# Kernel tuning notes

Hardware: AMD Instinct MI355X
Metric: run time of the kernel (lower is better)

## Reference

```python
import jax, jax.numpy as jnp
import numpy as np

N_NODES = 100000
N_EDGES = 1600000
IN_CH = 128
HID = 128
EPS = 1e-5


def setup_inputs() -> dict:
    key = jax.random.key(0)
    ks = jax.random.split(key, 16)
    x = jax.random.normal(ks[0], (N_NODES, IN_CH), dtype=jnp.float32)
    edge_index = jax.random.randint(ks[1], (2, N_EDGES), 0, N_NODES, dtype=jnp.int64)
    dims = [(IN_CH, HID), (HID, HID), (HID, HID // 2)]
    params = {}
    for i, (di, do) in enumerate(dims):
        params[f'w{i}'] = jax.random.normal(ks[2 + i], (di, do), dtype=jnp.float32) * (1.0 / np.sqrt(di))
        params[f'b{i}'] = jnp.zeros((do,), dtype=jnp.float32)
        params[f'g{i}'] = jnp.ones((do,), dtype=jnp.float32)
        params[f'be{i}'] = jnp.zeros((do,), dtype=jnp.float32)
    params['wc1'] = jax.random.normal(ks[8], (HID // 2, 32), dtype=jnp.float32) * (1.0 / np.sqrt(HID // 2))
    params['bc1'] = jnp.zeros((32,), dtype=jnp.float32)
    params['wc2'] = jax.random.normal(ks[9], (32, 1), dtype=jnp.float32) * (1.0 / np.sqrt(32))
    params['bc2'] = jnp.zeros((1,), dtype=jnp.float32)
    return {'x': x, 'edge_index': edge_index, **params}


def _gcn_forward(x, edge_index, w0, b0, g0, be0, w1, b1, g1, be1, w2, b2, g2, be2, wc1, bc1, wc2, bc2):
    n = x.shape[0]
    # add self-loops (GCNConv default)
    loops = jnp.arange(n, dtype=edge_index.dtype)
    src = jnp.concatenate([edge_index[0], loops])  # [E+N]
    dst = jnp.concatenate([edge_index[1], loops])
    # symmetric normalization: deg over targets (incl. self loops)
    deg = jax.ops.segment_sum(jnp.ones_like(dst, dtype=x.dtype), dst, num_segments=n)
    dis = jax.lax.rsqrt(jnp.maximum(deg, 1e-12))  # deg>=1 due to self loops
    norm = (dis[src] * dis[dst])[:, None]  # [E+N, 1]

    def layer(h, w, b, g, be):
        h = h @ w                                   # [N, d_out]
        h = jax.ops.segment_sum(h[src] * norm, dst, num_segments=n) + b
        mu = jnp.mean(h, axis=0)
        var = jnp.mean(jnp.square(h - mu), axis=0)  # biased var (torch BN)
        h = (h - mu) * jax.lax.rsqrt(var + EPS) * g + be
        return jax.nn.relu(h)                       # dropout: identity (eval)

    h = layer(x, w0, b0, g0, be0)
    h = layer(h, w1, b1, g1, be1)
    h = layer(h, w2, b2, g2, be2)
    h = jax.nn.relu(h @ wc1 + bc1)
    return (h @ wc2 + bc2)[:, 0]  # [N]


def reference(x, edge_index, w0, b0, g0, be0, w1, b1, g1, be1, w2, b2, g2, be2, wc1, bc1, wc2, bc2):
    return _gcn_forward(x, edge_index, w0, b0, g0, be0, w1, b1, g1, be1, w2, b2, g2, be2, wc1, bc1, wc2, bc2)
```

## Files before the change

kernel.cpp:

```cpp
#include <hip/hip_runtime.h>


typedef __attribute__((ext_vector_type(8))) short short8;
typedef __attribute__((ext_vector_type(4))) float f32x4;

#define BIN_SHIFT 7
#define BIN_NODES 128
#define CAPB 4096
#define SUBCAP 512
#define CAP 64
#define SPARTS 1024

__device__ __forceinline__ float b2f(unsigned short u) {
    return __uint_as_float(((unsigned)u) << 16);
}
__device__ __forceinline__ unsigned short f2bf(float f) {
    unsigned u = __float_as_uint(f);
    return (unsigned short)((u + 0x7fff + ((u >> 16) & 1)) >> 16);
}

__global__ __launch_bounds__(256) void part1_kernel(const int* __restrict__ eidx,
                                                    int E, int nbins, int chunk,
                                                    int* __restrict__ bin_fill,
                                                    int* __restrict__ binned) {
    __shared__ int cntS[1024];
    __shared__ int baseS[1024];
    int tid = threadIdx.x;
    int sub = blockIdx.x & 7;
    for (int b = tid; b < nbins; b += 256) cntS[b] = 0;
    __syncthreads();
    int e0 = blockIdx.x * chunk;
    int e1 = min(e0 + chunk, E);
    for (int e = e0 + tid; e < e1; e += 256)
        atomicAdd(&cntS[eidx[E + e] >> BIN_SHIFT], 1);
    __syncthreads();
    for (int b = tid; b < nbins; b += 256) {
        baseS[b] = atomicAdd(&bin_fill[b * 8 + sub], cntS[b]);
        cntS[b] = 0;
    }
    __syncthreads();
    for (int e = e0 + tid; e < e1; e += 256) {
        int d = eidx[E + e];
        int s = eidx[e];
        int b = d >> BIN_SHIFT;
        int p = baseS[b] + atomicAdd(&cntS[b], 1);
        if (p < SUBCAP)
            binned[b * CAPB + sub * SUBCAP + p] = (s << BIN_SHIFT) | (d & (BIN_NODES - 1));
    }
}

__global__ __launch_bounds__(256) void part2_kernel(const int* __restrict__ bin_fill,
                                                    const int* __restrict__ binned,
                                                    int N, int* __restrict__ fill,
                                                    float* __restrict__ dis,
                                                    int* __restrict__ stage) {
    __shared__ int lfill[BIN_NODES];
    int b = blockIdx.x, tid = threadIdx.x;
    if (tid < BIN_NODES) lfill[tid] = 0;
    __syncthreads();
    for (int sub = 0; sub < 8; sub++) {
        int cnt = min(bin_fill[b * 8 + sub], SUBCAP);
        const int* seg = binned + b * CAPB + sub * SUBCAP;
        for (int i = tid; i < cnt; i += 256) {
            int v = seg[i];
            int dl = v & (BIN_NODES - 1);
            int p = atomicAdd(&lfill[dl], 1);
            int node = (b << BIN_SHIFT) + dl;
            if (p < CAP) stage[(node << 6) + p] = v >> BIN_SHIFT;
        }
    }
    __syncthreads();
    if (tid < BIN_NODES) {
        int node = (b << BIN_SHIFT) + tid;
        if (node < N) {
            int c = lfill[tid];
            fill[node] = c;
            dis[node] = rsqrtf((float)c + 1.0f);
        }
    }
}

__global__ void wfrag_kernel(const float* __restrict__ w0,
                             const float* __restrict__ w1,
                             const float* __restrict__ w2,
                             unsigned short* __restrict__ wf) {
    int tid = blockIdx.x * 256 + threadIdx.x;
    if (tid >= 40960) return;
    const float* w;
    int idx, C;
    if (tid < 16384) { w = w0; idx = tid; C = 128; }
    else if (tid < 32768) { w = w1; idx = tid - 16384; C = 128; }
    else { w = w2; idx = tid - 32768; C = 64; }
    int j = idx & 7;
    int lane = (idx >> 3) & 63;
    int q = (idx >> 9) & 3;
    int n_tile = idx >> 11;
    int k = q * 32 + (lane >> 4) * 8 + j;
    int n = n_tile * 16 + (lane & 15);
    wf[tid] = f2bf(w[k * C + n]);
}

__device__ __forceinline__ void load8(const float* p, float4& lo, float4& hi) {
    lo = *(const float4*)p;
    hi = *(const float4*)(p + 4);
}
__device__ __forceinline__ void load8(const unsigned short* p, float4& lo, float4& hi) {
    int4 q = *(const int4*)p;
    lo = make_float4(__uint_as_float((unsigned)q.x << 16),
                     __uint_as_float((unsigned)q.x & 0xffff0000u),
                     __uint_as_float((unsigned)q.y << 16),
                     __uint_as_float((unsigned)q.y & 0xffff0000u));
    hi = make_float4(__uint_as_float((unsigned)q.z << 16),
                     __uint_as_float((unsigned)q.z & 0xffff0000u),
                     __uint_as_float((unsigned)q.w << 16),
                     __uint_as_float((unsigned)q.w & 0xffff0000u));
}

template <int C, typename InT>
__global__ __launch_bounds__(256, 5) void mfma_gemm_kernel(
    const InT* __restrict__ xin, const unsigned short* __restrict__ wf,
    const float* __restrict__ scale, const float* __restrict__ shift,
    const float* __restrict__ dis, unsigned short* __restrict__ out, int N) {
    constexpr int NT = C / 16;
    constexpr int WFRAGS = NT * 4 * 64;
    __shared__ short8 ws[WFRAGS];
    int tid = threadIdx.x;
    for (int i = tid; i < WFRAGS; i += 256) ws[i] = ((const short8*)wf)[i];

    int lane = tid & 63;
    int wave = tid >> 6;
    int m0 = blockIdx.x * 64 + wave * 16;
    int r15 = lane & 15, r4 = lane >> 4;
    f32x4 acc[NT];
#pragma unroll
    for (int t = 0; t < NT; t++) acc[t] = (f32x4){0.f, 0.f, 0.f, 0.f};
    int row0 = m0 + r15;
    int row0c = min(row0, N - 1);
    __syncthreads();

#pragma unroll
    for (int q = 0; q < 4; q++) {
        int kb = q * 32 + r4 * 8;
        float4 a0l, a0h;
        load8(xin + (size_t)row0c * 128 + kb, a0l, a0h);
        if (scale) {
            float4 scl = *(const float4*)&scale[kb];
            float4 sch = *(const float4*)&scale[kb + 4];
            float4 shl = *(const float4*)&shift[kb];
            float4 shh = *(const float4*)&shift[kb + 4];
            a0l.x = fmaxf(a0l.x * scl.x + shl.x, 0.f);
            a0l.y = fmaxf(a0l.y * scl.y + shl.y, 0.f);
            a0l.z = fmaxf(a0l.z * scl.z + shl.z, 0.f);
            a0l.w = fmaxf(a0l.w * scl.w + shl.w, 0.f);
            a0h.x = fmaxf(a0h.x * sch.x + shh.x, 0.f);
            a0h.y = fmaxf(a0h.y * sch.y + shh.y, 0.f);
            a0h.z = fmaxf(a0h.z * sch.z + shh.z, 0.f);
            a0h.w = fmaxf(a0h.w * sch.w + shh.w, 0.f);
        }
        short8 a0;
        a0[0] = (short)f2bf(a0l.x); a0[1] = (short)f2bf(a0l.y);
        a0[2] = (short)f2bf(a0l.z); a0[3] = (short)f2bf(a0l.w);
        a0[4] = (short)f2bf(a0h.x); a0[5] = (short)f2bf(a0h.y);
        a0[6] = (short)f2bf(a0h.z); a0[7] = (short)f2bf(a0h.w);
#pragma unroll
        for (int nt = 0; nt < NT; nt++) {
            short8 b = ws[(nt * 4 + q) * 64 + lane];
            acc[nt] = __builtin_amdgcn_mfma_f32_16x16x32_bf16(a0, b, acc[nt], 0, 0, 0);
        }
    }
    float d0r[4];
#pragma unroll
    for (int r = 0; r < 4; r++) {
        int rowa = m0 + r4 * 4 + r;
        d0r[r] = (rowa < N) ? dis[rowa] : 0.f;
    }
#pragma unroll
    for (int nt = 0; nt < NT; nt++) {
        int col = nt * 16 + r15;
#pragma unroll
        for (int r = 0; r < 4; r++) {
            int rowa = m0 + r4 * 4 + r;
            if (rowa < N) out[(size_t)rowa * C + col] = f2bf(acc[nt][r] * d0r[r]);
        }
    }
}

__global__ __launch_bounds__(256) void agg128_kernel(
    const unsigned short* __restrict__ h, const int* __restrict__ fill,
    const int* __restrict__ stage, const float* __restrict__ dis,
    unsigned short* __restrict__ out, int N) {
    int lane = threadIdx.x & 63;
    int node = blockIdx.x * 4 + (threadIdx.x >> 6);
    if (node >= N) return;
    float dn = dis[node];
    ushort2 sv = ((const ushort2*)(h + (size_t)node * 128))[lane];
    float2 acc = make_float2(b2f(sv.x), b2f(sv.y));
    int ne = min(fill[node], CAP);
    int pk = (lane < ne) ? stage[(node << 6) + lane] : 0;
    int j = 0;
    for (; j + 16 <= ne; j += 16) {
        ushort2 a[16];
#pragma unroll
        for (int t = 0; t < 16; t++) {
            int s = __builtin_amdgcn_readlane(pk, j + t);
            a[t] = ((const ushort2*)(h + (size_t)s * 128))[lane];
        }
#pragma unroll
        for (int t = 0; t < 16; t++) { acc.x += b2f(a[t].x); acc.y += b2f(a[t].y); }
    }
    for (; j + 8 <= ne; j += 8) {
        ushort2 a[8];
#pragma unroll
        for (int t = 0; t < 8; t++) {
            int s = __builtin_amdgcn_readlane(pk, j + t);
            a[t] = ((const ushort2*)(h + (size_t)s * 128))[lane];
        }
#pragma unroll
        for (int t = 0; t < 8; t++) { acc.x += b2f(a[t].x); acc.y += b2f(a[t].y); }
    }
    for (; j + 4 <= ne; j += 4) {
        ushort2 a[4];
#pragma unroll
        for (int t = 0; t < 4; t++) {
            int s = __builtin_amdgcn_readlane(pk, j + t);
            a[t] = ((const ushort2*)(h + (size_t)s * 128))[lane];
        }
#pragma unroll
        for (int t = 0; t < 4; t++) { acc.x += b2f(a[t].x); acc.y += b2f(a[t].y); }
    }
    for (; j < ne; j++) {
        int s = __builtin_amdgcn_readlane(pk, j);
        ushort2 a = ((const ushort2*)(h + (size_t)s * 128))[lane];
        acc.x += b2f(a.x);
        acc.y += b2f(a.y);
    }
    ((ushort2*)(out + (size_t)node * 128))[lane] =
        make_ushort2(f2bf(acc.x * dn), f2bf(acc.y * dn));
}

__global__ __launch_bounds__(256) void agg64_kernel(
    const unsigned short* __restrict__ h, const int* __restrict__ fill,
    const int* __restrict__ stage, const float* __restrict__ dis,
    unsigned short* __restrict__ out, int N) {
    int lane = threadIdx.x & 63;
    int node = blockIdx.x * 4 + (threadIdx.x >> 6);
    if (node >= N) return;
    int half = lane >> 5, ch = lane & 31;
    float dn = dis[node];
    float2 acc = make_float2(0.f, 0.f);
    if (half == 0) {
        ushort2 sv = ((const ushort2*)(h + (size_t)node * 64))[ch];
        acc.x = b2f(sv.x);
        acc.y = b2f(sv.y);
    }
    int ne = min(fill[node], CAP);
    int pk = (lane < ne) ? stage[(node << 6) + lane] : 0;
    int j = 0;
    for (; j + 16 <= ne; j += 16) {
        ushort2 a[8];
#pragma unroll
        for (int t = 0; t < 8; t++) {
            int s = __shfl(pk, j + 2 * t + half);
            a[t] = ((const ushort2*)(h + (size_t)s * 64))[ch];
        }
#pragma unroll
        for (int t = 0; t < 8; t++) { acc.x += b2f(a[t].x); acc.y += b2f(a[t].y); }
    }
    for (; j + 8 <= ne; j += 8) {
        ushort2 a[4];
#pragma unroll
        for (int t = 0; t < 4; t++) {
            int s = __shfl(pk, j + 2 * t + half);
            a[t] = ((const ushort2*)(h + (size_t)s * 64))[ch];
        }
#pragma unroll
        for (int t = 0; t < 4; t++) { acc.x += b2f(a[t].x); acc.y += b2f(a[t].y); }
    }
    for (; j < ne; j += 2) {
        int jj = j + half;
        int s = __shfl(pk, jj);
        bool v = jj < ne;
        ushort2 a = ((const ushort2*)(h + (size_t)s * 64))[ch];
        acc.x += v ? b2f(a.x) : 0.f;
        acc.y += v ? b2f(a.y) : 0.f;
    }
    acc.x += __shfl_down(acc.x, 32);
    acc.y += __shfl_down(acc.y, 32);
    if (half == 0)
        ((ushort2*)(out + (size_t)node * 64))[ch] =
            make_ushort2(f2bf(acc.x * dn), f2bf(acc.y * dn));
}

template <int C>
__global__ __launch_bounds__(256) void stats1_kernel(const unsigned short* __restrict__ h,
                                                     int N, float* __restrict__ partials) {
    constexpr int CG = C / 4;
    constexpr int RG = 256 / CG;
    int t = threadIdx.x;
    int cg = t % CG;
    int rg = t / CG;
    float s[4] = {0.f, 0.f, 0.f, 0.f}, q[4] = {0.f, 0.f, 0.f, 0.f};
    for (int n = blockIdx.x * RG + rg; n < N; n += gridDim.x * RG) {
        ushort4 v = *(const ushort4*)&h[(size_t)n * C + cg * 4];
        float f0 = b2f(v.x), f1 = b2f(v.y), f2 = b2f(v.z), f3 = b2f(v.w);
        s[0] += f0; s[1] += f1; s[2] += f2; s[3] += f3;
        q[0] += f0 * f0; q[1] += f1 * f1; q[2] += f2 * f2; q[3] += f3 * f3;
    }
    __shared__ float red[256 * 8];
#pragma unroll
    for (int k = 0; k < 4; k++) {
        red[(rg * CG + cg) * 8 + k] = s[k];
        red[(rg * CG + cg) * 8 + 4 + k] = q[k];
    }
    __syncthreads();
    if (rg == 0) {
#pragma unroll
        for (int w = 1; w < RG; w++)
#pragma unroll
            for (int k = 0; k < 4; k++) {
                s[k] += red[(w * CG + cg) * 8 + k];
                q[k] += red[(w * CG + cg) * 8 + 4 + k];
            }
        float* pb = partials + (size_t)blockIdx.x * 2 * C;
#pragma unroll
        for (int k = 0; k < 4; k++) {
            pb[cg * 4 + k] = s[k];
            pb[C + cg * 4 + k] = q[k];
        }
    }
}

template <int C>
__global__ __launch_bounds__(256) void stats2_kernel(const float* __restrict__ partials,
                                                     const float* __restrict__ g,
                                                     const float* __restrict__ be, int N,
                                                     float* __restrict__ scale,
                                                     float* __restrict__ shift) {
    int c = blockIdx.x;
    int t = threadIdx.x;
    float s = 0.f, q = 0.f;
    for (int b = t; b < SPARTS; b += 256) {
        const float* pb = partials + (size_t)b * 2 * C;
        s += pb[c];
        q += pb[C + c];
    }
    __shared__ float rs[256], rq[256];
    rs[t] = s;
    rq[t] = q;
    __syncthreads();
    for (int d = 128; d > 0; d >>= 1) {
        if (t < d) {
            rs[t] += rs[t + d];
            rq[t] += rq[t + d];
        }
        __syncthreads();
    }
    if (t == 0) {
        float inv_n = 1.0f / (float)N;
        float mean = rs[0] * inv_n;
        float var = rq[0] * inv_n - mean * mean;
        var = var > 0.f ? var : 0.f;
        float sc = g[c] * rsqrtf(var + 1e-5f);
        scale[c] = sc;
        shift[c] = be[c] - mean * sc;
    }
}

__global__ __launch_bounds__(256) void head_kernel(
    const unsigned short* __restrict__ h, const float* __restrict__ scale,
    const float* __restrict__ shift, const float* __restrict__ wc1,
    const float* __restrict__ bc1, const float* __restrict__ wc2,
    const float* __restrict__ bc2, float* __restrict__ out, int N) {
    __shared__ float w1s[64 * 32];
    __shared__ float b1s[32], w2s[32], s2s[64], sh2[64];
    __shared__ float b2s;
    int tid = threadIdx.x;
    for (int i = tid; i < 64 * 32; i += 256) w1s[i] = wc1[i];
    if (tid < 32) { b1s[tid] = bc1[tid]; w2s[tid] = wc2[tid]; }
    if (tid < 64) { s2s[tid] = scale[tid]; sh2[tid] = shift[tid]; }
    if (tid == 0) b2s = bc2[0];
    __syncthreads();
    int n = blockIdx.x * 256 + tid;
    if (n >= N) return;
    float v[64];
#pragma unroll
    for (int k = 0; k < 64; k++) {
        float x = b2f(h[(size_t)n * 64 + k]) * s2s[k] + sh2[k];
        v[k] = x > 0.f ? x : 0.f;
    }
    float o = b2s;
#pragma unroll 2
    for (int j = 0; j < 32; j++) {
        float t = b1s[j];
#pragma unroll
        for (int k = 0; k < 64; k++) t += v[k] * w1s[k * 32 + j];
        t = t > 0.f ? t : 0.f;
        o += t * w2s[j];
    }
    out[n] = o;
}

extern "C" void kernel_launch(void* const* d_in, const int* in_sizes, int n_in,
                              void* d_out, int out_size, void* d_ws, size_t ws_size,
                              hipStream_t stream) {
    const float* x = (const float*)d_in[0];
    const int* eidx = (const int*)d_in[1];
    const float* w0 = (const float*)d_in[2];
    const float* g0 = (const float*)d_in[4];
    const float* be0 = (const float*)d_in[5];
    const float* w1 = (const float*)d_in[6];
    const float* g1 = (const float*)d_in[8];
    const float* be1 = (const float*)d_in[9];
    const float* w2 = (const float*)d_in[10];
    const float* g2 = (const float*)d_in[12];
    const float* be2 = (const float*)d_in[13];
    const float* wc1 = (const float*)d_in[14];
    const float* bc1 = (const float*)d_in[15];
    const float* wc2 = (const float*)d_in[16];
    const float* bc2 = (const float*)d_in[17];

    const int N = in_sizes[0] / 128;
    const int E = in_sizes[1] / 2;
    const int nbins = (N + BIN_NODES - 1) >> BIN_SHIFT;

    char* p = (char*)d_ws;
    auto alloc = [&](size_t bytes) {
        void* r = (void*)p;
        p += (bytes + 255) & ~(size_t)255;
        return r;
    };
    int* bin_fill = (int*)alloc((size_t)nbins * 8 * 4);
    size_t zero_bytes = (size_t)(p - (char*)d_ws);
    int* fill = (int*)alloc((size_t)N * 4);
    int* binned = (int*)alloc((size_t)nbins * CAPB * 4);
    int* stage = (int*)alloc((size_t)N * CAP * 4);
    float* dis = (float*)alloc((size_t)N * 4);
    float* ss = (float*)alloc(3 * 256 * 4);
    float* partials = (float*)alloc((size_t)SPARTS * 256 * 4);
    unsigned short* hA = (unsigned short*)alloc((size_t)N * 128 * 2);
    unsigned short* hB = (unsigned short*)alloc((size_t)N * 128 * 2);
    unsigned short* wf = (unsigned short*)alloc(40960 * 2);
    unsigned short* wf0 = wf;
    unsigned short* wf1 = wf + 16384;
    unsigned short* wf2 = wf + 32768;

    float* sc0 = ss, *sh0 = ss + 128;
    float* sc1 = ss + 256, *sh1 = ss + 384;
    float* sc2 = ss + 512, *sh2 = ss + 640;

    hipMemsetAsync(d_ws, 0, zero_bytes, stream);

    wfrag_kernel<<<160, 256, 0, stream>>>(w0, w1, w2, wf);
    int p1_blocks = 256;
    int chunk = (E + p1_blocks - 1) / p1_blocks;
    part1_kernel<<<p1_blocks, 256, 0, stream>>>(eidx, E, nbins, chunk, bin_fill, binned);
    part2_kernel<<<nbins, 256, 0, stream>>>(bin_fill, binned, N, fill, dis, stage);

    int agg_grid = (N + 3) / 4;
    int gemm_grid = (N + 63) / 64;

    mfma_gemm_kernel<128, float><<<gemm_grid, 256, 0, stream>>>(x, wf0, nullptr, nullptr,
                                                                dis, hA, N);
    agg128_kernel<<<agg_grid, 256, 0, stream>>>(hA, fill, stage, dis, hB, N);
    stats1_kernel<128><<<SPARTS, 256, 0, stream>>>(hB, N, partials);
    stats2_kernel<128><<<128, 256, 0, stream>>>(partials, g0, be0, N, sc0, sh0);

    mfma_gemm_kernel<128, unsigned short><<<gemm_grid, 256, 0, stream>>>(
        hB, wf1, sc0, sh0, dis, hA, N);
    agg128_kernel<<<agg_grid, 256, 0, stream>>>(hA, fill, stage, dis, hB, N);
    stats1_kernel<128><<<SPARTS, 256, 0, stream>>>(hB, N, partials);
    stats2_kernel<128><<<128, 256, 0, stream>>>(partials, g1, be1, N, sc1, sh1);

    mfma_gemm_kernel<64, unsigned short><<<gemm_grid, 256, 0, stream>>>(
        hB, wf2, sc1, sh1, dis, hA, N);
    agg64_kernel<<<agg_grid, 256, 0, stream>>>(hA, fill, stage, dis, hB, N);
    stats1_kernel<64><<<SPARTS, 256, 0, stream>>>(hB, N, partials);
    stats2_kernel<64><<<64, 256, 0, stream>>>(partials, g2, be2, N, sc2, sh2);

    head_kernel<<<(N + 255) / 256, 256, 0, stream>>>(hB, sc2, sh2, wc1, bc1, wc2,
                                                     bc2, (float*)d_out, N);
}
```

Before: 435.4 us.

## Merge prep kernels, fuse BN stats reduction via last-block counter, widen agg blocks

Merges the weight-fragment conversion into the edge binning kernel as extra blocks, and fuses the two-pass BN statistics reduction into a single kernel in which the last block to finish (tracked by an atomic counter) does the final reduction. This removes several kernel launches. The partial count drops from 1024 to 256, aggregation blocks grow from 4 to 8 nodes (512 threads), and the head kernel now loads its bf16 input in vector chunks. The final reduction runs serially per channel in one block, and the fused stats step relies on threadfence ordering being correct.

Result: slower. 517.8 us (+18.9%).

```diff
diff --git a/kernel.cpp b/kernel.cpp
--- a/kernel.cpp
+++ b/kernel.cpp
@@ -9,7 +9,7 @@
 #define CAPB 4096
 #define SUBCAP 512
 #define CAP 64
-#define SPARTS 1024
+#define SPARTS 256
 
 __device__ __forceinline__ float b2f(unsigned short u) {
     return __uint_as_float(((unsigned)u) << 16);
@@ -19,17 +19,36 @@
     return (unsigned short)((u + 0x7fff + ((u >> 16) & 1)) >> 16);
 }
 
-__global__ __launch_bounds__(256) void part1_kernel(const int* __restrict__ eidx,
-                                                    int E, int nbins, int chunk,
-                                                    int* __restrict__ bin_fill,
-                                                    int* __restrict__ binned) {
+__global__ __launch_bounds__(256) void prep_kernel(
+    const float* __restrict__ w0, const float* __restrict__ w1,
+    const float* __restrict__ w2, unsigned short* __restrict__ wf,
+    const int* __restrict__ eidx, int E, int nbins, int chunk,
+    int* __restrict__ bin_fill, int* __restrict__ binned) {
     __shared__ int cntS[1024];
     __shared__ int baseS[1024];
+    if (blockIdx.x < 160) {
+        int tid = blockIdx.x * 256 + threadIdx.x;
+        if (tid >= 40960) return;
+        const float* w;
+        int idx, C;
+        if (tid < 16384) { w = w0; idx = tid; C = 128; }
+        else if (tid < 32768) { w = w1; idx = tid - 16384; C = 128; }
+        else { w = w2; idx = tid - 32768; C = 64; }
+        int j = idx & 7;
+        int lane = (idx >> 3) & 63;
+        int q = (idx >> 9) & 3;
+        int n_tile = idx >> 11;
+        int k = q * 32 + (lane >> 4) * 8 + j;
+        int n = n_tile * 16 + (lane & 15);
+        wf[tid] = f2bf(w[k * C + n]);
+        return;
+    }
+    int blk = blockIdx.x - 160;
     int tid = threadIdx.x;
-    int sub = blockIdx.x & 7;
+    int sub = blk & 7;
     for (int b = tid; b < nbins; b += 256) cntS[b] = 0;
     __syncthreads();
-    int e0 = blockIdx.x * chunk;
+    int e0 = blk * chunk;
     int e1 = min(e0 + chunk, E);
     for (int e = e0 + tid; e < e1; e += 256)
         atomicAdd(&cntS[eidx[E + e] >> BIN_SHIFT], 1);
@@ -78,26 +97,6 @@
             dis[node] = rsqrtf((float)c + 1.0f);
         }
     }
-}
-
-__global__ void wfrag_kernel(const float* __restrict__ w0,
-                             const float* __restrict__ w1,
-                             const float* __restrict__ w2,
-                             unsigned short* __restrict__ wf) {
-    int tid = blockIdx.x * 256 + threadIdx.x;
-    if (tid >= 40960) return;
-    const float* w;
-    int idx, C;
-    if (tid < 16384) { w = w0; idx = tid; C = 128; }
-    else if (tid < 32768) { w = w1; idx = tid - 16384; C = 128; }
-    else { w = w2; idx = tid - 32768; C = 64; }
-    int j = idx & 7;
-    int lane = (idx >> 3) & 63;
-    int q = (idx >> 9) & 3;
-    int n_tile = idx >> 11;
-    int k = q * 32 + (lane >> 4) * 8 + j;
-    int n = n_tile * 16 + (lane & 15);
-    wf[tid] = f2bf(w[k * C + n]);
 }
 
 __device__ __forceinline__ void load8(const float* p, float4& lo, float4& hi) {
@@ -185,12 +184,12 @@
     }
 }
 
-__global__ __launch_bounds__(256) void agg128_kernel(
+__global__ __launch_bounds__(512) void agg128_kernel(
     const unsigned short* __restrict__ h, const int* __restrict__ fill,
     const int* __restrict__ stage, const float* __restrict__ dis,
     unsigned short* __restrict__ out, int N) {
     int lane = threadIdx.x & 63;
-    int node = blockIdx.x * 4 + (threadIdx.x >> 6);
+    int node = blockIdx.x * 8 + (threadIdx.x >> 6);
     if (node >= N) return;
     float dn = dis[node];
     ushort2 sv = ((const ushort2*)(h + (size_t)node * 128))[lane];
@@ -238,12 +237,12 @@
         make_ushort2(f2bf(acc.x * dn), f2bf(acc.y * dn));
 }
 
-__global__ __launch_bounds__(256) void agg64_kernel(
+__global__ __launch_bounds__(512) void agg64_kernel(
     const unsigned short* __restrict__ h, const int* __restrict__ fill,
     const int* __restrict__ stage, const float* __restrict__ dis,
     unsigned short* __restrict__ out, int N) {
     int lane = threadIdx.x & 63;
-    int node = blockIdx.x * 4 + (threadIdx.x >> 6);
+    int node = blockIdx.x * 8 + (threadIdx.x >> 6);
     if (node >= N) return;
     int half = lane >> 5, ch = lane & 31;
     float dn = dis[node];
@@ -292,15 +291,18 @@
 }
 
 template <int C>
-__global__ __launch_bounds__(256) void stats1_kernel(const unsigned short* __restrict__ h,
-                                                     int N, float* __restrict__ partials) {
+__global__ __launch_bounds__(256) void stats_kernel(
+    const unsigned short* __restrict__ h, int N, float* __restrict__ partials,
+    unsigned int* __restrict__ counter, const float* __restrict__ g,
+    const float* __restrict__ be, float* __restrict__ scale,
+    float* __restrict__ shift) {
     constexpr int CG = C / 4;
     constexpr int RG = 256 / CG;
     int t = threadIdx.x;
     int cg = t % CG;
     int rg = t / CG;
     float s[4] = {0.f, 0.f, 0.f, 0.f}, q[4] = {0.f, 0.f, 0.f, 0.f};
-    for (int n = blockIdx.x * RG + rg; n < N; n += gridDim.x * RG) {
+    for (int n = blockIdx.x * RG + rg; n < N; n += SPARTS * RG) {
         ushort4 v = *(const ushort4*)&h[(size_t)n * C + cg * 4];
         float f0 = b2f(v.x), f1 = b2f(v.y), f2 = b2f(v.z), f3 = b2f(v.w);
         s[0] += f0; s[1] += f1; s[2] += f2; s[3] += f3;
@@ -328,41 +330,29 @@
             pb[C + cg * 4 + k] = q[k];
         }
     }
-}
-
-template <int C>
-__global__ __launch_bounds__(256) void stats2_kernel(const float* __restrict__ partials,
-                                                     const float* __restrict__ g,
-                                                     const float* __restrict__ be, int N,
-                                                     float* __restrict__ scale,
-                                                     float* __restrict__ shift) {
-    int c = blockIdx.x;
-    int t = threadIdx.x;
-    float s = 0.f, q = 0.f;
-    for (int b = t; b < SPARTS; b += 256) {
-        const float* pb = partials + (size_t)b * 2 * C;
-        s += pb[c];
-        q += pb[C + c];
-    }
-    __shared__ float rs[256], rq[256];
-    rs[t] = s;
-    rq[t] = q;
-    __syncthreads();
-    for (int d = 128; d > 0; d >>= 1) {
-        if (t < d) {
-            rs[t] += rs[t + d];
-            rq[t] += rq[t + d];
-        }
-        __syncthreads();
-    }
+    __threadfence();
+    __shared__ int lastS;
     if (t == 0) {
+        unsigned int old = atomicAdd(counter, 1u);
+        lastS = (old == (unsigned)(SPARTS - 1)) ? 1 : 0;
+    }
+    __syncthreads();
+    if (!lastS) return;
+    __threadfence();
+    if (t < C) {
+        float ss = 0.f, qq = 0.f;
+        for (int b = 0; b < SPARTS; b++) {
+            const float* pb = partials + (size_t)b * 2 * C;
+            ss += pb[t];
+            qq += pb[C + t];
+        }
         float inv_n = 1.0f / (float)N;
-        float mean = rs[0] * inv_n;
-        float var = rq[0] * inv_n - mean * mean;
+        float mean = ss * inv_n;
+        float var = qq * inv_n - mean * mean;
         var = var > 0.f ? var : 0.f;
-        float sc = g[c] * rsqrtf(var + 1e-5f);
-        scale[c] = sc;
-        shift[c] = be[c] - mean * sc;
+        float sc = g[t] * rsqrtf(var + 1e-5f);
+        scale[t] = sc;
+        shift[t] = be[t] - mean * sc;
     }
 }
 
@@ -384,9 +374,18 @@
     if (n >= N) return;
     float v[64];
 #pragma unroll
-    for (int k = 0; k < 64; k++) {
-        float x = b2f(h[(size_t)n * 64 + k]) * s2s[k] + sh2[k];
-        v[k] = x > 0.f ? x : 0.f;
+    for (int g8 = 0; g8 < 8; g8++) {
+        int4 raw = *(const int4*)&h[(size_t)n * 64 + g8 * 8];
+        unsigned rr[4] = {(unsigned)raw.x, (unsigned)raw.y, (unsigned)raw.z,
+                          (unsigned)raw.w};
+#pragma unroll
+        for (int k = 0; k < 4; k++) {
+            int c0 = g8 * 8 + k * 2;
+            float x0 = __uint_as_float(rr[k] << 16) * s2s[c0] + sh2[c0];
+            float x1 = __uint_as_float(rr[k] & 0xffff0000u) * s2s[c0 + 1] + sh2[c0 + 1];
+            v[c0] = x0 > 0.f ? x0 : 0.f;
+            v[c0 + 1] = x1 > 0.f ? x1 : 0.f;
+        }
     }
     float o = b2s;
 #pragma unroll 2
@@ -430,6 +429,7 @@
         return r;
     };
     int* bin_fill = (int*)alloc((size_t)nbins * 8 * 4);
+    unsigned int* counters = (unsigned int*)alloc(3 * 4);
     size_t zero_bytes = (size_t)(p - (char*)d_ws);
     int* fill = (int*)alloc((size_t)N * 4);
     int* binned = (int*)alloc((size_t)nbins * CAPB * 4);
@@ -450,32 +450,32 @@
 
     hipMemsetAsync(d_ws, 0, zero_bytes, stream);
 
-    wfrag_kernel<<<160, 256, 0, stream>>>(w0, w1, w2, wf);
     int p1_blocks = 256;
     int chunk = (E + p1_blocks - 1) / p1_blocks;
-    part1_kernel<<<p1_blocks, 256, 0, stream>>>(eidx, E, nbins, chunk, bin_fill, binned);
+    prep_kernel<<<160 + p1_blocks, 256, 0, stream>>>(w0, w1, w2, wf, eidx, E, nbins,
+                                                     chunk, bin_fill, binned);
     part2_kernel<<<nbins, 256, 0, stream>>>(bin_fill, binned, N, fill, dis, stage);
 
-    int agg_grid = (N + 3) / 4;
+    int agg_grid = (N + 7) / 8;
     int gemm_grid = (N + 63) / 64;
 
     mfma_gemm_kernel<128, float><<<gemm_grid, 256, 0, stream>>>(x, wf0, nullptr, nullptr,
                                                                 dis, hA, N);
-    agg128_kernel<<<agg_grid, 256, 0, stream>>>(hA, fill, stage, dis, hB, N);
-    stats1_kernel<128><<<SPARTS, 256, 0, stream>>>(hB, N, partials);
-    stats2_kernel<128><<<128, 256, 0, stream>>>(partials, g0, be0, N, sc0, sh0);
+    agg128_kernel<<<agg_grid, 512, 0, stream>>>(hA, fill, stage, dis, hB, N);
+    stats_kernel<128><<<SPARTS, 256, 0, stream>>>(hB, N, partials, counters + 0, g0, be0,
+                                                  sc0, sh0);
 
     mfma_gemm_kernel<128, unsigned short><<<gemm_grid, 256, 0, stream>>>(
         hB, wf1, sc0, sh0, dis, hA, N);
-    agg128_kernel<<<agg_grid, 256, 0, stream>>>(hA, fill, stage, dis, hB, N);
-    stats1_kernel<128><<<SPARTS, 256, 0, stream>>>(hB, N, partials);
-    stats2_kernel<128><<<128, 256, 0, stream>>>(partials, g1, be1, N, sc1, sh1);
+    agg128_kernel<<<agg_grid, 512, 0, stream>>>(hA, fill, stage, dis, hB, N);
+    stats_kernel<128><<<SPARTS, 256, 0, stream>>>(hB, N, partials, counters + 1, g1, be1,
+                                                  sc1, sh1);
 
     mfma_gemm_kernel<64, unsigned short><<<gemm_grid, 256, 0, stream>>>(
         hB, wf2, sc1, sh1, dis, hA, N);
-    agg64_kernel<<<agg_grid, 256, 0, stream>>>(hA, fill, stage, dis, hB, N);
-    stats1_kernel<64><<<SPARTS, 256, 0, stream>>>(hB, N, partials);
-    stats2_kernel<64><<<64, 256, 0, stream>>>(partials, g2, be2, N, sc2, sh2);
+    agg64_kernel<<<agg_grid, 512, 0, stream>>>(hA, fill, stage, dis, hB, N);
+    stats_kernel<64><<<SPARTS, 256, 0, stream>>>(hB, N, partials, counters + 2, g2, be2,
+                                                 sc2, sh2);
 
     head_kernel<<<(N + 255) / 256, 256, 0, stream>>>(hB, sc2, sh2, wc1, bc1, wc2,
                                                      bc2, (float*)d_out, N);
```
